# Performance work log

Measured on AMD Instinct MI355X. Metric: run time of the kernel, lower is better.

The kernel has to match this reference:

```python
import jax, jax.numpy as jnp
import numpy as np

BIT_SHIFT = 4
PROJECT = True
DIMS = [4096, 4096, 4096, 4096]
BATCH = 8192


def ternarize(w):
    # Ternary weight quantization {-1,0,+1} with straight-through estimator.
    q = jnp.clip(jnp.round(w), -1.0, 1.0)
    return w + jax.lax.stop_gradient(q - w)


def binarize(x):
    # Binary projection sign(x) with hardtanh straight-through estimator.
    c = jnp.clip(x, -1.0, 1.0)
    return c + jax.lax.stop_gradient(jnp.sign(x) - c)


def tern_bin_layer(x, w):
    # Ternary-weight matmul followed by bit-shift scaling (divide by 2**BIT_SHIFT),
    # then optional binary projection of the activation.
    scale = 1.0 / (1 << BIT_SHIFT)
    y = jnp.matmul(x, ternarize(w)) * scale
    if PROJECT:
        y = binarize(y)
    return y


def setup_inputs() -> dict:
    key = jax.random.key(0)
    ks = jax.random.split(key, 4)
    x = jax.random.normal(ks[0], (BATCH, DIMS[0]), dtype=jnp.float32)
    # Latent float weights; ternarized inside the layer.
    W0 = jax.random.normal(ks[1], (DIMS[0], DIMS[1]), dtype=jnp.float32) * 0.7
    W1 = jax.random.normal(ks[2], (DIMS[1], DIMS[2]), dtype=jnp.float32) * 0.7
    W2 = jax.random.normal(ks[3], (DIMS[2], DIMS[3]), dtype=jnp.float32) * 0.7
    return {"x": x, "W0": W0, "W1": W1, "W2": W2}


def reference(x, W0, W1, W2):
    h = tern_bin_layer(x, W0)
    h = tern_bin_layer(h, W1)
    h = tern_bin_layer(h, W2)
    return h
```

## Files before the change

kernel.cpp:

```cpp
#include <hip/hip_runtime.h>
#include <stdint.h>

#define MDIM 8192
#define KDIM 4096
#define NDIM 4096
#define MAXFLAGS (2 * 1024 * 1024)

typedef int i32x4 __attribute__((ext_vector_type(4)));

__device__ __forceinline__ void gl2lds16(const void* g, void* l) {
  __builtin_amdgcn_global_load_lds(
      (const __attribute__((address_space(1))) void*)(uintptr_t)(g),
      (__attribute__((address_space(3))) void*)(uintptr_t)(l), 16, 0, 0);
}

__global__ __launch_bounds__(256) void k_tern(const float* __restrict__ W,
                                              int8_t* __restrict__ Qt) {
  __shared__ int8_t t[64][65];
  const int n0 = blockIdx.x * 64;
  const int k0 = blockIdx.y * 64;
  const int tid = threadIdx.x;
  const int c = tid & 63;
  const int r0 = tid >> 6;
#pragma unroll
  for (int i = 0; i < 16; ++i) {
    int r = (i << 2) + r0;
    float w = W[(size_t)(k0 + r) * NDIM + (n0 + c)];
    float q = fminf(1.f, fmaxf(-1.f, rintf(w)));
    t[r][c] = (int8_t)(int)q;
  }
  __syncthreads();
#pragma unroll
  for (int i = 0; i < 16; ++i) {
    int r = (i << 2) + r0;
    Qt[(size_t)(n0 + r) * KDIM + (k0 + c)] = t[c][r];
  }
}

__global__ __launch_bounds__(256) void k_quant(const float* __restrict__ x,
                                               int8_t* __restrict__ dig) {
  const size_t P = (size_t)MDIM * KDIM;
  size_t i = ((size_t)blockIdx.x * 256 + threadIdx.x) * 4;
  float4 v = *(const float4*)(x + i);
  float f[4] = {v.x, v.y, v.z, v.w};
  int8_t dd[3][4];
#pragma unroll
  for (int j = 0; j < 4; ++j) {
    long long s = __double2ll_rn((double)f[j] * 524288.0);
    int8_t d0 = (int8_t)s; s = (s - d0) >> 8;
    int8_t d1 = (int8_t)s; s = (s - d1) >> 8;
    int8_t d2 = (int8_t)s;
    dd[0][j] = d0; dd[1][j] = d1; dd[2][j] = d2;
  }
#pragma unroll
  for (int p = 0; p < 3; ++p) {
    char4 c4; c4.x = dd[p][0]; c4.y = dd[p][1]; c4.z = dd[p][2]; c4.w = dd[p][3];
    *(char4*)(dig + p * P + i) = c4;
  }
}

__global__ void k_zero(int* c) {
  if (threadIdx.x == 0 && blockIdx.x == 0) *c = 0;
}

__global__ __launch_bounds__(512) void k_gemm_l1(const int8_t* __restrict__ dig,
                                                 const int8_t* __restrict__ Qt,
                                                 int8_t* __restrict__ h,
                                                 int* __restrict__ cnt,
                                                 int2* __restrict__ flags) {
  __shared__ __align__(16) int8_t As[3][64][128];
  __shared__ __align__(16) int8_t Bs[128][128];
  const int tid = threadIdx.x;
  const int w = tid >> 6, l = tid & 63;
  const size_t P = (size_t)MDIM * KDIM;

  const int nwg = gridDim.x;
  const int wg = (blockIdx.x & 7) * (nwg >> 3) + (blockIdx.x >> 3);
  const int NB = NDIM / 128;
  const int mb = wg / NB, nb = wg % NB;

  const int srow = tid >> 3;
  const int sswz = (tid & 7) ^ (srow & 7);
  const int8_t* a_src = dig + (size_t)(mb * 64 + srow) * KDIM + sswz * 16;
  const int8_t* b_src0 = Qt + (size_t)(nb * 128 + srow) * KDIM + sswz * 16;
  const int8_t* b_src1 = b_src0 + (size_t)64 * KDIM;
  int8_t* a_dst = &As[0][0][0] + w * 1024;
  int8_t* b_dst = &Bs[0][0] + w * 1024;

  i32x4 acc[3][2][2];
#pragma unroll
  for (int p = 0; p < 3; ++p)
#pragma unroll
    for (int mi = 0; mi < 2; ++mi)
#pragma unroll
      for (int ni = 0; ni < 2; ++ni) acc[p][mi][ni] = (i32x4){0, 0, 0, 0};

  const int wr = (w >> 2) * 32;
  const int wc = (w & 3) * 32;

  for (int kk = 0; kk < KDIM; kk += 128) {
#pragma unroll
    for (int p = 0; p < 3; ++p) gl2lds16(a_src + p * P + kk, a_dst + p * 8192);
    gl2lds16(b_src0 + kk, b_dst);
    gl2lds16(b_src1 + kk, b_dst + 8192);
    __syncthreads();
#pragma unroll
    for (int ki = 0; ki < 2; ++ki) {
      const int kg = ki * 4 + (l >> 4);
      i32x4 b[2];
#pragma unroll
      for (int ni = 0; ni < 2; ++ni) {
        int nr = wc + ni * 16 + (l & 15);
        b[ni] = *(const i32x4*)&Bs[nr][(kg ^ (nr & 7)) * 16];
      }
#pragma unroll
      for (int p = 0; p < 3; ++p)
#pragma unroll
        for (int mi = 0; mi < 2; ++mi) {
          int ar = wr + mi * 16 + (l & 15);
          i32x4 a = *(const i32x4*)&As[p][ar][(kg ^ (ar & 7)) * 16];
#pragma unroll
          for (int ni = 0; ni < 2; ++ni)
            acc[p][mi][ni] =
                __builtin_amdgcn_mfma_i32_16x16x64_i8(a, b[ni], acc[p][mi][ni], 0, 0, 0);
        }
    }
    __syncthreads();
  }

  const int mbase = mb * 64 + wr + ((l >> 4) << 2);
  const int nbase = nb * 128 + wc + (l & 15);
#pragma unroll
  for (int mi = 0; mi < 2; ++mi)
#pragma unroll
    for (int ni = 0; ni < 2; ++ni)
#pragma unroll
      for (int j = 0; j < 4; ++j) {
        int s0 = acc[0][mi][ni][j], s1 = acc[1][mi][ni][j];
        int s2 = acc[2][mi][ni][j];
        double d = ((double)s2 * 256.0 + (double)s1) * 256.0 + (double)s0;
        int sg = (d > 0.0) - (d < 0.0);
        int row = mbase + mi * 16 + j;
        int col = nbase + ni * 16;
        h[(size_t)row * NDIM + col] = (int8_t)sg;
        if (fabs(d) <= 2048.0) {
          int idx = atomicAdd(cnt, 1);
          if (idx < MAXFLAGS) flags[idx] = make_int2(row, col);
        }
      }
}

__global__ __launch_bounds__(256) void k_fixup(const float* __restrict__ x,
                                               const int8_t* __restrict__ Qt,
                                               const int* __restrict__ cnt,
                                               const int2* __restrict__ flags,
                                               int8_t* __restrict__ h) {
  __shared__ double red[256];
  int n = *cnt;
  if (n > MAXFLAGS) n = MAXFLAGS;
  for (int i = blockIdx.x; i < n; i += gridDim.x) {
    int2 rc = flags[i];
    const float* xr = x + (size_t)rc.x * KDIM;
    const int8_t* qr = Qt + (size_t)rc.y * KDIM;
    double s = 0.0;
    for (int k = threadIdx.x; k < KDIM; k += 256)
      s += (double)xr[k] * (double)qr[k];
    red[threadIdx.x] = s;
    __syncthreads();
#pragma unroll
    for (int st = 128; st > 0; st >>= 1) {
      if (threadIdx.x < st) red[threadIdx.x] += red[threadIdx.x + st];
      __syncthreads();
    }
    if (threadIdx.x == 0) {
      double d = red[0];
      h[(size_t)rc.x * NDIM + rc.y] = (int8_t)((d > 0.0) - (d < 0.0));
    }
    __syncthreads();
  }
}

template <int F32OUT>
__global__ __launch_bounds__(512) void k_gemm_bin(const int8_t* __restrict__ A,
                                                  const int8_t* __restrict__ Qt,
                                                  void* __restrict__ outp) {
  __shared__ __align__(16) int8_t As[128][128];
  __shared__ __align__(16) int8_t Bs[128][128];
  const int tid = threadIdx.x;
  const int w = tid >> 6, l = tid & 63;

  const int nwg = gridDim.x;
  const int wg = (blockIdx.x & 7) * (nwg >> 3) + (blockIdx.x >> 3);
  const int NB = NDIM / 128;
  const int mb = wg / NB, nb = wg % NB;

  const int srow = tid >> 3;
  const int sswz = (tid & 7) ^ (srow & 7);
  const int8_t* a0 = A + (size_t)(mb * 128 + srow) * KDIM + sswz * 16;
  const int8_t* a1 = a0 + (size_t)64 * KDIM;
  const int8_t* b0 = Qt + (size_t)(nb * 128 + srow) * KDIM + sswz * 16;
  const int8_t* b1 = b0 + (size_t)64 * KDIM;
  int8_t* a_dst = &As[0][0] + w * 1024;
  int8_t* b_dst = &Bs[0][0] + w * 1024;

  i32x4 acc[4][2];
#pragma unroll
  for (int mi = 0; mi < 4; ++mi)
#pragma unroll
    for (int ni = 0; ni < 2; ++ni) acc[mi][ni] = (i32x4){0, 0, 0, 0};

  const int wr = (w >> 2) * 64, wc = (w & 3) * 32;

  for (int kk = 0; kk < KDIM; kk += 128) {
    gl2lds16(a0 + kk, a_dst);
    gl2lds16(a1 + kk, a_dst + 8192);
    gl2lds16(b0 + kk, b_dst);
    gl2lds16(b1 + kk, b_dst + 8192);
    __syncthreads();
#pragma unroll
    for (int ki = 0; ki < 2; ++ki) {
      const int kg = ki * 4 + (l >> 4);
      i32x4 b[2];
#pragma unroll
      for (int ni = 0; ni < 2; ++ni) {
        int nr = wc + ni * 16 + (l & 15);
        b[ni] = *(const i32x4*)&Bs[nr][(kg ^ (nr & 7)) * 16];
      }
#pragma unroll
      for (int mi = 0; mi < 4; ++mi) {
        int ar = wr + mi * 16 + (l & 15);
        i32x4 a = *(const i32x4*)&As[ar][(kg ^ (ar & 7)) * 16];
#pragma unroll
        for (int ni = 0; ni < 2; ++ni)
          acc[mi][ni] = __builtin_amdgcn_mfma_i32_16x16x64_i8(a, b[ni], acc[mi][ni], 0, 0, 0);
      }
    }
    __syncthreads();
  }

  const int mbase = mb * 128 + wr + ((l >> 4) << 2);
  const int nbase = nb * 128 + wc + (l & 15);
#pragma unroll
  for (int mi = 0; mi < 4; ++mi)
#pragma unroll
    for (int ni = 0; ni < 2; ++ni)
#pragma unroll
      for (int j = 0; j < 4; ++j) {
        int s = acc[mi][ni][j];
        int sg = (s > 0) - (s < 0);
        size_t off = (size_t)(mbase + mi * 16 + j) * NDIM + (nbase + ni * 16);
        if (F32OUT)
          ((float*)outp)[off] = (float)sg;
        else
          ((int8_t*)outp)[off] = (int8_t)sg;
      }
}

extern "C" void kernel_launch(void* const* d_in, const int* in_sizes, int n_in,
                              void* d_out, int out_size, void* d_ws, size_t ws_size,
                              hipStream_t stream) {
  (void)in_sizes; (void)n_in; (void)out_size; (void)ws_size;
  const float* x  = (const float*)d_in[0];
  const float* W0 = (const float*)d_in[1];
  const float* W1 = (const float*)d_in[2];
  const float* W2 = (const float*)d_in[3];
  float* out = (float*)d_out;

  const size_t QB = (size_t)KDIM * NDIM;
  const size_t HB = (size_t)MDIM * NDIM;
  int8_t* Qt0 = (int8_t*)d_ws;
  int8_t* Qt1 = Qt0 + QB;
  int8_t* Qt2 = Qt1 + QB;
  int8_t* h0  = Qt2 + QB;
  int8_t* h1  = h0 + HB;

  int8_t* dig = (int8_t*)d_out;
  int2* flags = (int2*)((char*)d_out + 3 * HB);
  int* cnt = (int*)((char*)d_out + 3 * HB + (size_t)MAXFLAGS * 8);

  dim3 tgrid(NDIM / 64, KDIM / 64);
  k_tern<<<tgrid, 256, 0, stream>>>(W0, Qt0);
  k_tern<<<tgrid, 256, 0, stream>>>(W1, Qt1);
  k_tern<<<tgrid, 256, 0, stream>>>(W2, Qt2);
  k_quant<<<((size_t)MDIM * KDIM) / 1024, 256, 0, stream>>>(x, dig);
  k_zero<<<1, 64, 0, stream>>>(cnt);
  k_gemm_l1<<<(MDIM / 64) * (NDIM / 128), 512, 0, stream>>>(dig, Qt0, h0, cnt, flags);
  k_fixup<<<512, 256, 0, stream>>>(x, Qt0, cnt, flags, h0);
  k_gemm_bin<0><<<(MDIM / 128) * (NDIM / 128), 512, 0, stream>>>(h0, Qt1, h1);
  k_gemm_bin<1><<<(MDIM / 128) * (NDIM / 128), 512, 0, stream>>>(h1, Qt2, out);
}
```

Before: 795.3 us.

## Double-buffer LDS tiles in int8 GEMM kernels to overlap loads with MFMA

Both GEMM kernels now keep two LDS buffers and prefetch the tile two steps ahead with global_load_lds. Explicit vmcnt/lgkmcnt waits and raw s_barrier calls replace the per-tile __syncthreads pair, so global-to-LDS transfers overlap MFMA compute. Wave priority is also raised around the MFMA block. This doubles LDS use per block (up to 80KB in the layer-1 kernel), which may reduce occupancy, and the hand-written waitcnt counts must match the number of outstanding loads to stay correct.

```diff
diff --git a/kernel.cpp b/kernel.cpp
--- a/kernel.cpp
+++ b/kernel.cpp
@@ -68,8 +68,8 @@
                                                  int8_t* __restrict__ h,
                                                  int* __restrict__ cnt,
                                                  int2* __restrict__ flags) {
-  __shared__ __align__(16) int8_t As[3][64][128];
-  __shared__ __align__(16) int8_t Bs[128][128];
+  __shared__ __align__(16) int8_t As[2][3][64][128];
+  __shared__ __align__(16) int8_t Bs[2][128][128];
   const int tid = threadIdx.x;
   const int w = tid >> 6, l = tid & 63;
   const size_t P = (size_t)MDIM * KDIM;
@@ -84,8 +84,6 @@
   const int8_t* a_src = dig + (size_t)(mb * 64 + srow) * KDIM + sswz * 16;
   const int8_t* b_src0 = Qt + (size_t)(nb * 128 + srow) * KDIM + sswz * 16;
   const int8_t* b_src1 = b_src0 + (size_t)64 * KDIM;
-  int8_t* a_dst = &As[0][0][0] + w * 1024;
-  int8_t* b_dst = &Bs[0][0] + w * 1024;
 
   i32x4 acc[3][2][2];
 #pragma unroll
@@ -98,12 +96,16 @@
   const int wr = (w >> 2) * 32;
   const int wc = (w & 3) * 32;
 
-  for (int kk = 0; kk < KDIM; kk += 128) {
-#pragma unroll
-    for (int p = 0; p < 3; ++p) gl2lds16(a_src + p * P + kk, a_dst + p * 8192);
-    gl2lds16(b_src0 + kk, b_dst);
-    gl2lds16(b_src1 + kk, b_dst + 8192);
-    __syncthreads();
+  auto stage = [&](int buf, int kk) {
+    int8_t* ad = &As[buf][0][0][0] + w * 1024;
+    int8_t* bd = &Bs[buf][0][0] + w * 1024;
+#pragma unroll
+    for (int p = 0; p < 3; ++p) gl2lds16(a_src + p * P + kk, ad + p * 8192);
+    gl2lds16(b_src0 + kk, bd);
+    gl2lds16(b_src1 + kk, bd + 8192);
+  };
+
+  auto compute = [&](int buf) {
 #pragma unroll
     for (int ki = 0; ki < 2; ++ki) {
       const int kg = ki * 4 + (l >> 4);
@@ -111,21 +113,45 @@
 #pragma unroll
       for (int ni = 0; ni < 2; ++ni) {
         int nr = wc + ni * 16 + (l & 15);
-        b[ni] = *(const i32x4*)&Bs[nr][(kg ^ (nr & 7)) * 16];
-      }
+        b[ni] = *(const i32x4*)&Bs[buf][nr][(kg ^ (nr & 7)) * 16];
+      }
+      __builtin_amdgcn_s_setprio(1);
 #pragma unroll
       for (int p = 0; p < 3; ++p)
 #pragma unroll
         for (int mi = 0; mi < 2; ++mi) {
           int ar = wr + mi * 16 + (l & 15);
-          i32x4 a = *(const i32x4*)&As[p][ar][(kg ^ (ar & 7)) * 16];
+          i32x4 a = *(const i32x4*)&As[buf][p][ar][(kg ^ (ar & 7)) * 16];
 #pragma unroll
           for (int ni = 0; ni < 2; ++ni)
             acc[p][mi][ni] =
                 __builtin_amdgcn_mfma_i32_16x16x64_i8(a, b[ni], acc[p][mi][ni], 0, 0, 0);
         }
-    }
-    __syncthreads();
+      __builtin_amdgcn_s_setprio(0);
+    }
+  };
+
+  stage(0, 0);
+  stage(1, 128);
+  asm volatile("s_waitcnt vmcnt(5)" ::: "memory");
+  __builtin_amdgcn_sched_barrier(0);
+  __builtin_amdgcn_s_barrier();
+
+  const int NT = KDIM / 128;
+  for (int t = 0; t < NT; ++t) {
+    compute(t & 1);
+    if (t == NT - 1) break;
+    asm volatile("s_waitcnt lgkmcnt(0)" ::: "memory");
+    __builtin_amdgcn_sched_barrier(0);
+    __builtin_amdgcn_s_barrier();
+    if (t + 2 < NT) {
+      stage(t & 1, (t + 2) * 128);
+      asm volatile("s_waitcnt vmcnt(5)" ::: "memory");
+    } else {
+      asm volatile("s_waitcnt vmcnt(0)" ::: "memory");
+    }
+    __builtin_amdgcn_sched_barrier(0);
+    __builtin_amdgcn_s_barrier();
   }
 
   const int mbase = mb * 64 + wr + ((l >> 4) << 2);
@@ -184,8 +210,8 @@
 __global__ __launch_bounds__(512) void k_gemm_bin(const int8_t* __restrict__ A,
                                                   const int8_t* __restrict__ Qt,
                                                   void* __restrict__ outp) {
-  __shared__ __align__(16) int8_t As[128][128];
-  __shared__ __align__(16) int8_t Bs[128][128];
+  __shared__ __align__(16) int8_t As[2][128][128];
+  __shared__ __align__(16) int8_t Bs[2][128][128];
   const int tid = threadIdx.x;
   const int w = tid >> 6, l = tid & 63;
 
@@ -200,8 +226,6 @@
   const int8_t* a1 = a0 + (size_t)64 * KDIM;
   const int8_t* b0 = Qt + (size_t)(nb * 128 + srow) * KDIM + sswz * 16;
   const int8_t* b1 = b0 + (size_t)64 * KDIM;
-  int8_t* a_dst = &As[0][0] + w * 1024;
-  int8_t* b_dst = &Bs[0][0] + w * 1024;
 
   i32x4 acc[4][2];
 #pragma unroll
@@ -211,12 +235,16 @@
 
   const int wr = (w >> 2) * 64, wc = (w & 3) * 32;
 
-  for (int kk = 0; kk < KDIM; kk += 128) {
-    gl2lds16(a0 + kk, a_dst);
-    gl2lds16(a1 + kk, a_dst + 8192);
-    gl2lds16(b0 + kk, b_dst);
-    gl2lds16(b1 + kk, b_dst + 8192);
-    __syncthreads();
+  auto stage = [&](int buf, int kk) {
+    int8_t* ad = &As[buf][0][0] + w * 1024;
+    int8_t* bd = &Bs[buf][0][0] + w * 1024;
+    gl2lds16(a0 + kk, ad);
+    gl2lds16(a1 + kk, ad + 8192);
+    gl2lds16(b0 + kk, bd);
+    gl2lds16(b1 + kk, bd + 8192);
+  };
+
+  auto compute = [&](int buf) {
 #pragma unroll
     for (int ki = 0; ki < 2; ++ki) {
       const int kg = ki * 4 + (l >> 4);
@@ -224,18 +252,42 @@
 #pragma unroll
       for (int ni = 0; ni < 2; ++ni) {
         int nr = wc + ni * 16 + (l & 15);
-        b[ni] = *(const i32x4*)&Bs[nr][(kg ^ (nr & 7)) * 16];
-      }
+        b[ni] = *(const i32x4*)&Bs[buf][nr][(kg ^ (nr & 7)) * 16];
+      }
+      __builtin_amdgcn_s_setprio(1);
 #pragma unroll
       for (int mi = 0; mi < 4; ++mi) {
         int ar = wr + mi * 16 + (l & 15);
-        i32x4 a = *(const i32x4*)&As[ar][(kg ^ (ar & 7)) * 16];
+        i32x4 a = *(const i32x4*)&As[buf][ar][(kg ^ (ar & 7)) * 16];
 #pragma unroll
         for (int ni = 0; ni < 2; ++ni)
           acc[mi][ni] = __builtin_amdgcn_mfma_i32_16x16x64_i8(a, b[ni], acc[mi][ni], 0, 0, 0);
       }
-    }
-    __syncthreads();
+      __builtin_amdgcn_s_setprio(0);
+    }
+  };
+
+  stage(0, 0);
+  stage(1, 128);
+  asm volatile("s_waitcnt vmcnt(4)" ::: "memory");
+  __builtin_amdgcn_sched_barrier(0);
+  __builtin_amdgcn_s_barrier();
+
+  const int NT = KDIM / 128;
+  for (int t = 0; t < NT; ++t) {
+    compute(t & 1);
+    if (t == NT - 1) break;
+    asm volatile("s_waitcnt lgkmcnt(0)" ::: "memory");
+    __builtin_amdgcn_sched_barrier(0);
+    __builtin_amdgcn_s_barrier();
+    if (t + 2 < NT) {
+      stage(t & 1, (t + 2) * 128);
+      asm volatile("s_waitcnt vmcnt(4)" ::: "memory");
+    } else {
+      asm volatile("s_waitcnt vmcnt(0)" ::: "memory");
+    }
+    __builtin_amdgcn_sched_barrier(0);
+    __builtin_amdgcn_s_barrier();
   }
 
   const int mbase = mb * 128 + wr + ((l >> 4) << 2);
```

New measurement: 803.6 us. Within noise of the previous version (+1.0%).
